# Optimization experiments

Hardware: AMD Instinct MI355X
Metric: run time of the kernel (lower is better)

## Reference

```python
import jax, jax.numpy as jnp
import numpy as np

B, F, C, W_, H_ = 4, 8, 256, 7, 7   # batch, frames, compressed channels (in_dim//r), width, height
CIN = 2048                          # in_dim
CH = CIN // 16                      # in_dim // (2*r) = 128, per-branch q/k channels


def _pw2d(x, W, b):
    # 1x1 Conv2d == per-pixel channel matmul. x: (N,Cin,H,W), W: (Cout,Cin)
    return jnp.einsum('nchw,oc->nohw', x, W) + b[None, :, None, None]


def setup_inputs() -> dict:
    key = jax.random.key(0)
    ks = iter(jax.random.split(key, 40))
    def rn(shape, s=0.02):
        return jax.random.normal(next(ks), shape, dtype=jnp.float32) * s
    inp = {
        'x':       rn((B * F, CIN, H_, W_), 1.0),
        'domainX': rn((B * F, CIN, H_, W_), 1.0),
        'domainY': rn((B * F, 1, H_, W_), 1.0),
        # conv1_1_pre (1 -> 2048), output is discarded in forward but computed faithfully
        'w_pre': rn((CIN, 1)), 'b_pre': rn((CIN,)),
        # conv3 (2048 -> 256); its weight is SHARED with layer1_downconv and layer1_downconv_Y
        'w_conv3': rn((C, CIN)), 'b_conv3': rn((C,)),
        # value_conv 1x1x1 Conv3d (256 -> 2048); weight SHARED with layer1_upconv(_Y)
        'w_value': rn((CIN, C)), 'b_value': rn((CIN,)),
        # tied-weight convs have their own biases
        'b_l1down': rn((C,)), 'b_l1up': rn((CIN,)),
        'b_l1down_Y': rn((C,)), 'b_l1up_Y': rn((CIN,)),
        # layer2 convs: independent weights (layer2_*gamma init to 0, so init add is a no-op)
        'w_l2down': rn((C, CIN)), 'b_l2down': rn((C,)),
        'w_l2up': rn((CIN, C)), 'b_l2up': rn((CIN,)),
        'w_l2down_Y': rn((C, CIN)), 'b_l2down_Y': rn((C,)),
        'w_l2up_Y': rn((CIN, C)), 'b_l2up_Y': rn((CIN,)),
        # q/k projections (2048 -> 128 each)
        'w_c11': rn((CH, CIN)), 'b_c11': rn((CH,)),
        'w_c12': rn((CH, CIN)), 'b_c12': rn((CH,)),
        'w_c21': rn((CH, CIN)), 'b_c21': rn((CH,)),
        'w_c22': rn((CH, CIN)), 'b_c22': rn((CH,)),
        'pos_embedV': rn((1, F, C * H_ * W_), 1.0),
        'gamma': jnp.asarray(0.01, dtype=jnp.float32),
    }
    return inp


def reference(x, domainX, domainY, w_pre, b_pre, w_conv3, b_conv3, w_value, b_value,
              b_l1down, b_l1up, b_l1down_Y, b_l1up_Y,
              w_l2down, b_l2down, w_l2up, b_l2up,
              w_l2down_Y, b_l2down_Y, w_l2up_Y, b_l2up_Y,
              w_c11, b_c11, w_c12, b_c12, w_c21, b_c21, w_c22, b_c22,
              pos_embedV, gamma):
    S = F * W_ * H_  # 392 tokens per clip
    # conv1_1_pre output is overwritten in the original forward (dead computation)
    _dead = _pw2d(domainY, w_pre, b_pre)
    del _dead
    # domainY path: down(conv3 weight) -> up(value_conv weight) -> layer2 down -> layer2 up
    # (create5D/create4D + permutes + 1x1x1 conv3d collapse to pointwise channel matmuls)
    dY = _pw2d(_pw2d(_pw2d(_pw2d(domainX, w_conv3, b_l1down_Y), w_value, b_l1up_Y),
                     w_l2down_Y, b_l2down_Y), w_l2up_Y, b_l2up_Y)
    q4 = jnp.concatenate([_pw2d(x, w_c11, b_c11), _pw2d(dY, w_c12, b_c12)], axis=1)  # (32,256,7,7)
    q = q4.reshape(B, F, C, W_, H_).transpose(0, 1, 3, 4, 2).reshape(B, S, C)
    # domainX path (same structure, shared layer1 weights, its own biases)
    dX = _pw2d(_pw2d(_pw2d(_pw2d(domainX, w_conv3, b_l1down), w_value, b_l1up),
                     w_l2down, b_l2down), w_l2up, b_l2up)
    k4 = jnp.concatenate([_pw2d(x, w_c21, b_c21), _pw2d(dX, w_c22, b_c22)], axis=1)
    k5 = k4.reshape(B, F, C, W_, H_).transpose(0, 1, 3, 4, 2)        # (B,F,W,H,C)
    k = k5.transpose(0, 2, 1, 3, 4).reshape(B, C, S)                 # faithful odd permute
    # value: conv3 -> +pos_embed -> rearrange to (B, S, C)
    v4 = _pw2d(x, w_conv3, b_conv3)                                  # (32,256,7,7)
    v = v4.reshape(B, F, C * W_ * H_) + pos_embedV                   # dropout p=0 is identity
    v = v.reshape(B, F, C, W_, H_).transpose(0, 1, 3, 4, 2).reshape(B, S, C)
    attn = jax.nn.softmax(jnp.einsum('bnc,bcm->bnm', q, k), axis=-1)  # (B,392,392)
    out = jnp.einsum('bnm,bmc->bnc', attn, v)
    out = out.reshape(B, F, W_, H_, C).transpose(0, 4, 1, 2, 3)      # (B,C,F,W,H)
    out = jnp.einsum('bcthw,oc->bothw', out, w_value) + b_value[None, :, None, None, None]
    out = out.transpose(0, 2, 1, 3, 4).reshape(B * F, CIN, W_, H_)
    return (gamma * out + x) * out + x
```

## Files before the change

kernel.cpp:

```cpp
#include <hip/hip_runtime.h>
#include <hip/hip_bf16.h>


typedef __attribute__((ext_vector_type(8))) _Float16 half8;
typedef __attribute__((ext_vector_type(4))) float f32x4;

#define TOKENS 1568

__device__ __forceinline__ ushort f2h(float f) {
    _Float16 h = (_Float16)f;
    return *(ushort*)&h;
}
__device__ __forceinline__ float h2f(ushort u) {
    _Float16 h = *(_Float16*)&u;
    return (float)h;
}

__device__ __forceinline__ void gl16(const void* g, void* l) {
    __builtin_amdgcn_global_load_lds(
        (const __attribute__((address_space(1))) unsigned int*)g,
        (__attribute__((address_space(3))) unsigned int*)l, 16, 0, 0);
}

#define EPI_PART  0
#define EPI_F16   1
#define EPI_QK2   2
#define EPI_FINAL 3

struct GA {
    const ushort* Ah; int lda; long sA;
    const ushort* Wh; int ldw; long sW;
    const float* bias; int sB;
    int nkc, Kc;
    float* fO; ushort* bO; ushort* bO2;
    int ldc; long sC; int M, N;
    int nx, ny;
    const float *ex, *gamma; float* fout;
};

template<int EPI>
__device__ __forceinline__ void gmm_body(const GA g, int bx, int by, int bzf,
                                         ushort* LA, ushort* LW)
{
    const int tid = threadIdx.x;
    const int bz = bzf / g.nkc;
    const int kc = bzf % g.nkc;
    const int row0 = by * 64, col0 = bx * 128;

    const int srow = tid >> 2;
    const int sq   = (tid & 3) ^ (srow & 3);
    int am  = row0 + srow;      if (am  > g.M - 1) am  = g.M - 1;
    int wn0 = col0 + srow;      if (wn0 > g.N - 1) wn0 = g.N - 1;
    int wn1 = col0 + 64 + srow; if (wn1 > g.N - 1) wn1 = g.N - 1;
    const long kbase = (long)kc * g.Kc + sq * 8;
    const ushort* gA  = g.Ah + bz * g.sA + (long)am  * g.lda + kbase;
    const ushort* gW0 = g.Wh + bz * g.sW + (long)wn0 * g.ldw + kbase;
    const ushort* gW1 = g.Wh + bz * g.sW + (long)wn1 * g.ldw + kbase;
    const int wb = (tid & 192) * 8;

    auto STAGE = [&](int buf, int k0) {
        gl16(gA + k0, LA + buf * 2048 + wb);
        gl16(gW0 + k0, LW + buf * 4096 + wb);
        gl16(gW1 + k0, LW + buf * 4096 + 2048 + wb);
    };

    const int lane = tid & 63, wv = tid >> 6;
    const int wr = (wv >> 1) * 32, wc = (wv & 1) * 64;
    const int fr = lane & 15;
    const int ksw = ((lane >> 4) ^ (lane & 3)) * 8;
    int aoff[2], boff[4];
#pragma unroll
    for (int mi = 0; mi < 2; ++mi) aoff[mi] = (wr + mi * 16 + fr) * 32 + ksw;
#pragma unroll
    for (int ni = 0; ni < 4; ++ni) boff[ni] = (wc + ni * 16 + fr) * 32 + ksw;

    f32x4 acc[2][4];
#pragma unroll
    for (int mi = 0; mi < 2; ++mi)
#pragma unroll
        for (int ni = 0; ni < 4; ++ni) acc[mi][ni] = (f32x4){0.f, 0.f, 0.f, 0.f};

    STAGE(0, 0);
    __syncthreads();
    int cur = 0;
    for (int k0 = 0; k0 < g.Kc; k0 += 32) {
        if (k0 + 32 < g.Kc) STAGE(cur ^ 1, k0 + 32);

        half8 fa[2], fb[4];
#pragma unroll
        for (int mi = 0; mi < 2; ++mi) fa[mi] = *(half8*)&LA[cur * 2048 + aoff[mi]];
#pragma unroll
        for (int ni = 0; ni < 4; ++ni) fb[ni] = *(half8*)&LW[cur * 4096 + boff[ni]];
#pragma unroll
        for (int mi = 0; mi < 2; ++mi)
#pragma unroll
            for (int ni = 0; ni < 4; ++ni)
                acc[mi][ni] = __builtin_amdgcn_mfma_f32_16x16x32_f16(fa[mi], fb[ni], acc[mi][ni], 0, 0, 0);
        __syncthreads();
        cur ^= 1;
    }

    const int q4 = (lane >> 4) * 4;
    float gg = 0.f;
    if constexpr (EPI == EPI_FINAL) gg = g.gamma[0];
#pragma unroll
    for (int mi = 0; mi < 2; ++mi)
#pragma unroll
        for (int ni = 0; ni < 4; ++ni)
#pragma unroll
            for (int qi = 0; qi < 4; ++qi) {
                int m = row0 + wr + mi * 16 + q4 + qi;
                int n = col0 + wc + ni * 16 + fr;
                if (m >= g.M || n >= g.N) continue;
                float v = acc[mi][ni][qi];
                if (g.bias) v += g.bias[bz * g.sB + n];
                if constexpr (EPI == EPI_PART) {
                    g.fO[(long)bzf * g.sC + (long)m * g.ldc + n] = v;
                } else if constexpr (EPI == EPI_F16) {
                    g.bO[(long)bzf * g.sC + (long)m * g.ldc + n] = f2h(v);
                } else if constexpr (EPI == EPI_QK2) {
                    ushort h = f2h(v);
                    if (n < 128) {
                        int c = 128 + n;
                        int p = m % 49, img = m / 49, f = img & 7, b = img >> 3;
                        int flat = (p / 7) * 14336 + f * 1792 + (p % 7) * 256 + c;
                        int ci = flat / 392, mm = flat % 392;
                        g.bO2[(long)b * 100352 + (long)mm * 256 + ci] = h;
                    } else {
                        g.bO[m * 256 + n] = h;
                    }
                } else {
                    int nimg = m / 49, p = m % 49;
                    long xi = (long)nimg * (2048 * 49) + (long)n * 49 + p;
                    float xv = g.ex[xi];
                    g.fout[xi] = (gg * v + xv) * v + xv;
                }
            }
}

template<int EPI>
__global__ __launch_bounds__(256)
void gmm(GA g)
{
    __shared__ __align__(16) ushort LA[2 * 2048], LW[2 * 4096];
    gmm_body<EPI>(g, blockIdx.x, blockIdx.y, blockIdx.z, LA, LW);
}

__global__ __launch_bounds__(256)
void gmm4(GA g1, int n1, GA g2, int n2, GA g3, int n3, GA g4)
{
    __shared__ __align__(16) ushort LA[2 * 2048], LW[2 * 4096];
    int id = blockIdx.x;
    if (id < n1) {
        int bx = id % g1.nx, t = id / g1.nx;
        gmm_body<EPI_PART>(g1, bx, t % g1.ny, t / g1.ny, LA, LW);
    } else if (id < n1 + n2) {
        id -= n1;
        int bx = id % g2.nx, t = id / g2.nx;
        gmm_body<EPI_PART>(g2, bx, t % g2.ny, t / g2.ny, LA, LW);
    } else if (id < n1 + n2 + n3) {
        id -= n1 + n2;
        int bx = id % g3.nx, t = id / g3.nx;
        gmm_body<EPI_PART>(g3, bx, t % g3.ny, t / g3.ny, LA, LW);
    } else {
        id -= n1 + n2 + n3;
        int bx = id % g4.nx, t = id / g4.nx;
        gmm_body<EPI_PART>(g4, bx, t % g4.ny, t / g4.ny, LA, LW);
    }
}

__global__ __launch_bounds__(256)
void prep(const float* c11, const float* c21, const float* conv3,
          const float* c22, const float* c12, const float* wval,
          const float* w2dX, const float* w2dY,
          const float* b_c11, const float* b_c21, const float* b_conv3,
          const float* x, const float* dX,
          const float* w2u, const float* w2uY, const float* wv,
          ushort* Wg1, ushort* C2, ushort* Wval, ushort* W2dS, float* bg1,
          ushort* Xt, ushort* DXt,
          ushort* W2uT, ushort* WvT)
{
    __shared__ float tile[64][65];
    int b = blockIdx.x;
    int tid = threadIdx.x;
    if (b < 12290) {
        int e = b * 256 + tid;
        if (e < 1048576) {
            float v = e < 262144 ? c11[e] : e < 524288 ? c21[e - 262144] : conv3[e - 524288];
            Wg1[e] = f2h(v);
        } else if (e < 1572864) {
            int i = e - 1048576;
            C2[i] = f2h(i < 262144 ? c22[i] : c12[i - 262144]);
        } else if (e < 2097152) {
            int i = e - 1572864; Wval[i] = f2h(wval[i]);
        } else if (e < 2097664) {
            int i = e - 2097152;
            bg1[i] = i < 128 ? b_c11[i] : i < 256 ? b_c21[i - 128] : b_conv3[i - 256];
        } else {
            int i = e - 2097664;
            W2dS[i] = f2h(i < 524288 ? w2dX[i] : w2dY[i - 524288]);
        }
    } else if (b < 14338) {
        int local = b - 12290;
        int z = local >> 10;
        int rem = local & 1023;
        int n = rem & 31, c0 = (rem >> 5) * 64;
        const float* src = z ? dX : x;
        ushort* oh = z ? DXt : Xt;
        const float* s = src + (long)n * (2048 * 49) + (long)c0 * 49;
        for (int idx = tid; idx < 64 * 49; idx += 256)
            tile[idx / 49][idx % 49] = s[idx];
        __syncthreads();
        for (int idx = tid; idx < 49 * 64; idx += 256) {
            int p = idx >> 6, cl = idx & 63;
            long o = (long)(n * 49 + p) * 2048 + c0 + cl;
            oh[o] = f2h(tile[cl][p]);
        }
    } else {
        int local = b - 14338;
        int zc = local >> 7, t = local & 127;
        const float* src; ushort* dh;
        switch (zc) {
            case 0:  src = w2u;  dh = W2uT;          break;
            case 1:  src = w2uY; dh = W2uT + 524288; break;
            default: src = wv;   dh = WvT;           break;
        }
        const int rows = 2048, cols = 256;
        int tilesX = cols >> 6;
        int tx = t % tilesX, ty = t / tilesX;
        for (int i = tid; i < 4096; i += 256) {
            int r = i >> 6, c = i & 63;
            tile[r][c] = src[(long)(ty * 64 + r) * cols + tx * 64 + c];
        }
        __syncthreads();
        for (int i = tid; i < 4096; i += 256) {
            int c = i >> 6, r = i & 63;
            long o = (long)(tx * 64 + c) * rows + ty * 64 + r;
            dh[o] = f2h(tile[r][c]);
        }
    }
}

__global__ __launch_bounds__(256)
void redA(const float* __restrict__ PG1, const float* __restrict__ bg1,
          const float* __restrict__ pos,
          ushort* Q, ushort* Km, ushort* V,
          const float* __restrict__ A1p, ushort* A1,
          const float* __restrict__ Dp, ushort* DT,
          const float* __restrict__ P0p, ushort* P0,
          const float* w2dX, const float* w2dY,
          const float* b1dX, const float* b1uX, const float* b2dX,
          const float* b1dY, const float* b1uY, const float* b2dY,
          float* __restrict__ dvec)
{
    int blk = blockIdx.x, tid = threadIdx.x;
    if (blk < 3136) {
        int idx = blk * 256 + tid;
        int m = idx >> 9, n = idx & 511;
        float v = bg1[n];
#pragma unroll
        for (int k = 0; k < 8; ++k) v += PG1[(long)k * 802816 + idx];
        int p = m % 49, img = m / 49;
        int f = img & 7, b = img >> 3;
        if (n < 128) {
            Q[m * 256 + n] = f2h(v);
        } else if (n < 256) {
            int c = n - 128;
            int flat = (p / 7) * 14336 + f * 1792 + (p % 7) * 256 + c;
            int ci = flat / 392, mm = flat % 392;
            Km[(long)b * 100352 + (long)mm * 256 + ci] = f2h(v);
        } else {
            int c = n - 256;
            v += pos[f * 12544 + c * 49 + p];
            int s = m % 392;
            long o = (long)b * 106496 + (long)c * 416 + s;
            V[o] = f2h(v);
            if (s < 24) V[o + 392] = 0;
        }
    } else if (blk < 3200) {
        int b2 = blk - 3136;
#pragma unroll
        for (int r = 0; r < 4; ++r) {
            int idx = b2 * 1024 + r * 256 + tid;
            int z = idx >> 15, e = idx & 32767;
            float v = 0.f;
#pragma unroll
            for (int k = 0; k < 8; ++k) v += A1p[(long)(z * 8 + k) * 32768 + e];
            A1[idx] = f2h(v);
        }
    } else if (blk < 3232) {
        int b2 = blk - 3200;
#pragma unroll
        for (int r = 0; r < 16; ++r) {
            int idx = b2 * 4096 + r * 256 + tid;
            int z = idx >> 16, e = idx & 65535;
            int i = e >> 8, j = e & 255;
            float v = 0.f;
#pragma unroll
            for (int k = 0; k < 8; ++k) v += Dp[(long)(z * 8 + k) * 65536 + e];
            DT[(long)z * 65536 + (long)j * 256 + i] = f2h(v);
        }
    } else if (blk < 3360) {
        int blk2 = blk - 3232;
        int z = blk2 >> 6;
        int lane = tid & 63, wv = tid >> 6;
        int c = (blk2 & 63) * 4 + wv;
        const float* w2d = (z ? w2dY : w2dX) + (long)c * 2048;
        const float* b1d = z ? b1dY : b1dX;
        const float* b1u = z ? b1uY : b1uX;
        const float* b2d = z ? b2dY : b2dX;
        float acc = 0.f;
        for (int o = lane; o < 2048; o += 64) acc = fmaf(w2d[o], b1u[o], acc);
        for (int j = lane; j < 256; j += 64) {
            float d = 0.f;
#pragma unroll
            for (int k = 0; k < 8; ++k) d += Dp[(long)(z * 8 + k) * 65536 + (long)c * 256 + j];
            acc = fmaf(d, b1d[j], acc);
        }
        for (int off = 32; off; off >>= 1) acc += __shfl_down(acc, off, 64);
        if (lane == 0) dvec[z * 256 + c] = acc + b2d[c];
    } else {
        int idx = (blk - 3360) * 256 + tid;
        float v = 0.f;
#pragma unroll
        for (int k = 0; k < 4; ++k) v += P0p[(long)k * 401408 + idx];
        P0[idx] = f2h(v);
    }
}

__global__ __launch_bounds__(256)
void a3kc(GA gA3,
          const ushort* __restrict__ A1, const float* __restrict__ dvec,
          const float* c22, const float* c12,
          const float* b2uX, const float* b2uY,
          const float* bc22, const float* bc12, float* kc)
{
    __shared__ __align__(16) ushort LA[2 * 2048], LW[2 * 4096];
    int id = blockIdx.x;
    if (id < 8) {
        int bx = id & 1, t = id >> 1;
        gmm_body<EPI_F16>(gA3, bx, t & 1, t >> 1, LA, LW);
        return;
    }
    int tid = threadIdx.x, lane = tid & 63, wv = tid >> 6;
    int w = (id - 8) * 4 + wv;
    int z = w >> 7, i = w & 127;
    const ushort* a1 = A1 + (long)z * 32768 + i * 256;
    const float* dv = dvec + z * 256;
    const float* cr = (z ? c12 : c22) + (long)i * 2048;
    const float* b2u = z ? b2uY : b2uX;
    float acc = 0.f;
    for (int c = lane; c < 256; c += 64) acc = fmaf(h2f(a1[c]), dv[c], acc);
    for (int o = lane; o < 2048; o += 64) acc = fmaf(cr[o], b2u[o], acc);
    for (int off = 32; off; off >>= 1) acc += __shfl_down(acc, off, 64);
    if (lane == 0) kc[z * 128 + i] = acc + (z ? bc12 : bc22)[i];
}

__global__ __launch_bounds__(256)
void fattn(const ushort* __restrict__ Qg, const ushort* __restrict__ Kmg,
           const ushort* __restrict__ VT, ushort* __restrict__ O)
{
    __shared__ float raw[16 * 420];
    __shared__ ushort P[16 * 424];
    const int b = blockIdx.y;
    const int r0 = blockIdx.x * 16;
    const int tid = threadIdx.x;
    const int lane = tid & 63, wv = tid >> 6;
    const int fr = lane & 15, g = lane >> 4;
    const int kb = g * 8;
    const long base = (long)b * 100352;
    const long vbase = (long)b * 106496;

    int qr = r0 + fr; if (qr > 391) qr = 391;
    const ushort* qp = Qg + base + (long)qr * 256 + kb;
    half8 qh[8];
#pragma unroll
    for (int kf = 0; kf < 8; ++kf) qh[kf] = *(const half8*)(qp + kf * 32);

    for (int nf = wv; nf < 26; nf += 4) {
        int kcol = nf * 16 + fr; if (kcol > 391) kcol = 391;
        const ushort* kp = Kmg + base + (long)kcol * 256 + kb;
        f32x4 a = (f32x4){0.f, 0.f, 0.f, 0.f};
#pragma unroll
        for (int kf = 0; kf < 8; ++kf) {
            half8 bh = *(const half8*)(kp + kf * 32);
            a = __builtin_amdgcn_mfma_f32_16x16x32_f16(qh[kf], bh, a, 0, 0, 0);
        }
#pragma unroll
        for (int q = 0; q < 4; ++q)
            raw[(g * 4 + q) * 420 + nf * 16 + fr] = a[q];
    }
    __syncthreads();

    {
        int row = tid >> 4, j = tid & 15;
        float v[26];
        float m = -1e30f;
#pragma unroll
        for (int k = 0; k < 26; ++k) {
            int col = j + 16 * k;
            v[k] = (col < 392) ? raw[row * 420 + col] : -1e30f;
            m = fmaxf(m, v[k]);
        }
#pragma unroll
        for (int off = 8; off; off >>= 1) m = fmaxf(m, __shfl_xor(m, off, 16));
        float s = 0.f;
#pragma unroll
        for (int k = 0; k < 26; ++k) { v[k] = __expf(v[k] - m); s += v[k]; }
#pragma unroll
        for (int off = 8; off; off >>= 1) s += __shfl_xor(s, off, 16);
        float inv = 1.f / s;
#pragma unroll
        for (int k = 0; k < 26; ++k) {
            int col = j + 16 * k;
            P[row * 424 + col] = (col < 392) ? f2h(v[k] * inv) : (ushort)0;
        }
    }
    __syncthreads();

    const int cf0 = wv * 4;
    f32x4 o[4];
#pragma unroll
    for (int c = 0; c < 4; ++c) o[c] = (f32x4){0.f, 0.f, 0.f, 0.f};
#pragma unroll
    for (int kf = 0; kf < 13; ++kf) {
        half8 pa = *(half8*)&P[fr * 424 + kf * 32 + kb];
#pragma unroll
        for (int c = 0; c < 4; ++c) {
            const ushort* vp = VT + vbase + (long)((cf0 + c) * 16 + fr) * 416 + kf * 32 + kb;
            half8 vb = *(const half8*)vp;
            o[c] = __builtin_amdgcn_mfma_f32_16x16x32_f16(pa, vb, o[c], 0, 0, 0);
        }
    }
#pragma unroll
    for (int c = 0; c < 4; ++c)
#pragma unroll
        for (int q = 0; q < 4; ++q) {
            int orow = r0 + g * 4 + q;
            if (orow < 392)
                O[base + (long)orow * 256 + (cf0 + c) * 16 + fr] = f2h(o[c][q]);
        }
}

extern "C" void kernel_launch(void* const* d_in, const int* in_sizes, int n_in,
                              void* d_out, int out_size, void* d_ws, size_t ws_size,
                              hipStream_t stream)
{
    const float* x        = (const float*)d_in[0];
    const float* domainX  = (const float*)d_in[1];
    const float* w_conv3  = (const float*)d_in[5];
    const float* b_conv3  = (const float*)d_in[6];
    const float* w_value  = (const float*)d_in[7];
    const float* b_value  = (const float*)d_in[8];
    const float* b_l1down   = (const float*)d_in[9];
    const float* b_l1up     = (const float*)d_in[10];
    const float* b_l1down_Y = (const float*)d_in[11];
    const float* b_l1up_Y   = (const float*)d_in[12];
    const float* w_l2down   = (const float*)d_in[13];
    const float* b_l2down   = (const float*)d_in[14];
    const float* w_l2up     = (const float*)d_in[15];
    const float* b_l2up     = (const float*)d_in[16];
    const float* w_l2down_Y = (const float*)d_in[17];
    const float* b_l2down_Y = (const float*)d_in[18];
    const float* w_l2up_Y   = (const float*)d_in[19];
    const float* b_l2up_Y   = (const float*)d_in[20];
    const float* w_c11 = (const float*)d_in[21];
    const float* b_c11 = (const float*)d_in[22];
    const float* w_c12 = (const float*)d_in[23];
    const float* b_c12 = (const float*)d_in[24];
    const float* w_c21 = (const float*)d_in[25];
    const float* b_c21 = (const float*)d_in[26];
    const float* w_c22 = (const float*)d_in[27];
    const float* b_c22 = (const float*)d_in[28];
    const float* pos   = (const float*)d_in[29];
    const float* gamma = (const float*)d_in[30];
    float* out = (float*)d_out;

    ushort* U = (ushort*)d_ws;
    float*  Fp = (float*)d_ws;

    const long oXt   = 0;
    const long oDXt  = 3211264;
    const long oWg1  = 6422528;
    const long oWval = 7471104;
    const long oC2   = 7995392;
    const long oW2uT = 8519680;
    const long oWvT  = 9568256;
    const long oW2dS = 10092544;
    const long oQ    = 11141120;
    const long oKm   = 11542528;
    const long oVT   = 11943936;
    const long oA1   = 12369920;
    const long oDT   = 12435456;
    const long oA3   = 12566528;
    const long oP0   = 12632064;
    const long oO    = 13033472;
    const long fPG1  = 6979584;
    const long fP0p  = 13402112;
    const long fA1p  = 15007744;
    const long fDp   = 15532032;
    const long fbg1  = 16580608;
    const long fkc   = 16581120;
    const long fdv   = 16581376;

    GA Z = {};

    prep<<<dim3(14722), 256, 0, stream>>>(
        w_c11, w_c21, w_conv3, w_c22, w_c12, w_value, w_l2down, w_l2down_Y,
        b_c11, b_c21, b_conv3, x, domainX,
        w_l2up, w_l2up_Y, w_value,
        U + oWg1, U + oC2, U + oWval, U + oW2dS, Fp + fbg1,
        U + oXt, U + oDXt,
        U + oW2uT, U + oWvT);

    {
        GA g1 = Z;
        g1.Ah = U + oXt; g1.lda = 2048; g1.sA = 0;
        g1.Wh = U + oWg1; g1.ldw = 2048; g1.sW = 0;
        g1.nkc = 8; g1.Kc = 256; g1.fO = Fp + fPG1;
        g1.ldc = 512; g1.sC = 802816; g1.M = TOKENS; g1.N = 512; g1.nx = 4; g1.ny = 25;
        GA ga1 = Z;
        ga1.Ah = U + oC2; ga1.lda = 2048; ga1.sA = 262144;
        ga1.Wh = U + oW2uT; ga1.ldw = 2048; ga1.sW = 524288;
        ga1.nkc = 8; ga1.Kc = 256; ga1.fO = Fp + fA1p;
        ga1.ldc = 256; ga1.sC = 32768; ga1.M = 128; ga1.N = 256; ga1.nx = 2; ga1.ny = 2;
        GA gd = Z;
        gd.Ah = U + oW2dS; gd.lda = 2048; gd.sA = 524288;
        gd.Wh = U + oWvT; gd.ldw = 2048; gd.sW = 0;
        gd.nkc = 8; gd.Kc = 256; gd.fO = Fp + fDp;
        gd.ldc = 256; gd.sC = 65536; gd.M = 256; gd.N = 256; gd.nx = 2; gd.ny = 4;
        GA gp = Z;
        gp.Ah = U + oDXt; gp.lda = 2048; gp.sA = 0;
        gp.Wh = U + oWg1 + 524288; gp.ldw = 2048; gp.sW = 0;
        gp.nkc = 4; gp.Kc = 512; gp.fO = Fp + fP0p;
        gp.ldc = 256; gp.sC = 401408; gp.M = TOKENS; gp.N = 256; gp.nx = 2; gp.ny = 25;
        gmm4<<<dim3(1192), 256, 0, stream>>>(g1, 800, ga1, 64, gd, 128, gp);
    }

    redA<<<dim3(4928), 256, 0, stream>>>(Fp + fPG1, Fp + fbg1, pos,
        U + oQ, U + oKm, U + oVT,
        Fp + fA1p, U + oA1,
        Fp + fDp, U + oDT,
        Fp + fP0p, U + oP0,
        w_l2down, w_l2down_Y,
        b_l1down, b_l1up, b_l2down,
        b_l1down_Y, b_l1up_Y, b_l2down_Y,
        Fp + fdv);

    {
        GA g = Z;
        g.Ah = U + oA1; g.lda = 256; g.sA = 32768;
        g.Wh = U + oDT; g.ldw = 256; g.sW = 65536;
        g.nkc = 1; g.Kc = 256; g.bO = U + oA3;
        g.ldc = 256; g.sC = 32768; g.M = 128; g.N = 256; g.nx = 2; g.ny = 2;
        a3kc<<<dim3(72), 256, 0, stream>>>(g,
            U + oA1, Fp + fdv,
            w_c22, w_c12, b_l2up, b_l2up_Y,
            b_c22, b_c12, Fp + fkc);
    }

    {
        GA g = Z;
        g.Ah = U + oP0; g.lda = 256; g.sA = 0;
        g.Wh = U + oA3; g.ldw = 256; g.sW = 0;
        g.bias = Fp + fkc; g.sB = 0;
        g.nkc = 1; g.Kc = 256;
        g.bO = U + oQ; g.bO2 = U + oKm;
        g.ldc = 0; g.sC = 0; g.M = TOKENS; g.N = 256; g.nx = 2; g.ny = 25;
        gmm<EPI_QK2><<<dim3(2, 25, 1), 256, 0, stream>>>(g);
    }

    fattn<<<dim3(25, 4), 256, 0, stream>>>(U + oQ, U + oKm, U + oVT, U + oO);

    {
        GA g = Z;
        g.Ah = U + oO; g.lda = 256; g.sA = 0;
        g.Wh = U + oWval; g.ldw = 256; g.sW = 0;
        g.bias = b_value; g.sB = 0;
        g.nkc = 1; g.Kc = 256;
        g.ldc = 0; g.sC = 0; g.M = TOKENS; g.N = 2048; g.nx = 16; g.ny = 25;
        g.ex = x; g.gamma = gamma; g.fout = out;
        gmm<EPI_FINAL><<<dim3(16, 25, 1), 256, 0, stream>>>(g);
    }
}
```

Before: 147.8 us.

## Load GEMM fragments directly from global memory, dropping LDS staging

Removes the double-buffered LDS staging (global_load_lds plus barriers) from the shared GEMM body. Each lane now reads its MFMA A and B fragments straight from global memory. This drops the LDS allocation, so occupancy can rise, and eliminates the per-iteration __syncthreads. The cost is that no data is shared between waves: each wave re-fetches the tiles others also use, global accesses become less coalesced (16 B per row per lane), and load latency is no longer overlapped with compute by prefetch.

Result: slower. 174.3 us (+17.9%).

```diff
diff --git a/kernel.cpp b/kernel.cpp
--- a/kernel.cpp
+++ b/kernel.cpp
@@ -14,12 +14,6 @@
 __device__ __forceinline__ float h2f(ushort u) {
     _Float16 h = *(_Float16*)&u;
     return (float)h;
-}
-
-__device__ __forceinline__ void gl16(const void* g, void* l) {
-    __builtin_amdgcn_global_load_lds(
-        (const __attribute__((address_space(1))) unsigned int*)g,
-        (__attribute__((address_space(3))) unsigned int*)l, 16, 0, 0);
 }
 
 #define EPI_PART  0
@@ -39,40 +33,31 @@
 };
 
 template<int EPI>
-__device__ __forceinline__ void gmm_body(const GA g, int bx, int by, int bzf,
-                                         ushort* LA, ushort* LW)
+__device__ __forceinline__ void gmm_body(const GA g, int bx, int by, int bzf)
 {
     const int tid = threadIdx.x;
     const int bz = bzf / g.nkc;
     const int kc = bzf % g.nkc;
     const int row0 = by * 64, col0 = bx * 128;
 
-    const int srow = tid >> 2;
-    const int sq   = (tid & 3) ^ (srow & 3);
-    int am  = row0 + srow;      if (am  > g.M - 1) am  = g.M - 1;
-    int wn0 = col0 + srow;      if (wn0 > g.N - 1) wn0 = g.N - 1;
-    int wn1 = col0 + 64 + srow; if (wn1 > g.N - 1) wn1 = g.N - 1;
-    const long kbase = (long)kc * g.Kc + sq * 8;
-    const ushort* gA  = g.Ah + bz * g.sA + (long)am  * g.lda + kbase;
-    const ushort* gW0 = g.Wh + bz * g.sW + (long)wn0 * g.ldw + kbase;
-    const ushort* gW1 = g.Wh + bz * g.sW + (long)wn1 * g.ldw + kbase;
-    const int wb = (tid & 192) * 8;
-
-    auto STAGE = [&](int buf, int k0) {
-        gl16(gA + k0, LA + buf * 2048 + wb);
-        gl16(gW0 + k0, LW + buf * 4096 + wb);
-        gl16(gW1 + k0, LW + buf * 4096 + 2048 + wb);
-    };
-
     const int lane = tid & 63, wv = tid >> 6;
     const int wr = (wv >> 1) * 32, wc = (wv & 1) * 64;
     const int fr = lane & 15;
-    const int ksw = ((lane >> 4) ^ (lane & 3)) * 8;
-    int aoff[2], boff[4];
-#pragma unroll
-    for (int mi = 0; mi < 2; ++mi) aoff[mi] = (wr + mi * 16 + fr) * 32 + ksw;
-#pragma unroll
-    for (int ni = 0; ni < 4; ++ni) boff[ni] = (wc + ni * 16 + fr) * 32 + ksw;
+    const int kb = (lane >> 4) * 8;
+    const long kbase = (long)kc * g.Kc + kb;
+
+    const ushort* pa[2];
+#pragma unroll
+    for (int mi = 0; mi < 2; ++mi) {
+        int r = row0 + wr + mi * 16 + fr; if (r > g.M - 1) r = g.M - 1;
+        pa[mi] = g.Ah + bz * g.sA + (long)r * g.lda + kbase;
+    }
+    const ushort* pb[4];
+#pragma unroll
+    for (int ni = 0; ni < 4; ++ni) {
+        int c = col0 + wc + ni * 16 + fr; if (c > g.N - 1) c = g.N - 1;
+        pb[ni] = g.Wh + bz * g.sW + (long)c * g.ldw + kbase;
+    }
 
     f32x4 acc[2][4];
 #pragma unroll
@@ -80,24 +65,17 @@
 #pragma unroll
         for (int ni = 0; ni < 4; ++ni) acc[mi][ni] = (f32x4){0.f, 0.f, 0.f, 0.f};
 
-    STAGE(0, 0);
-    __syncthreads();
-    int cur = 0;
     for (int k0 = 0; k0 < g.Kc; k0 += 32) {
-        if (k0 + 32 < g.Kc) STAGE(cur ^ 1, k0 + 32);
-
         half8 fa[2], fb[4];
 #pragma unroll
-        for (int mi = 0; mi < 2; ++mi) fa[mi] = *(half8*)&LA[cur * 2048 + aoff[mi]];
-#pragma unroll
-        for (int ni = 0; ni < 4; ++ni) fb[ni] = *(half8*)&LW[cur * 4096 + boff[ni]];
+        for (int mi = 0; mi < 2; ++mi) fa[mi] = *(const half8*)(pa[mi] + k0);
+#pragma unroll
+        for (int ni = 0; ni < 4; ++ni) fb[ni] = *(const half8*)(pb[ni] + k0);
 #pragma unroll
         for (int mi = 0; mi < 2; ++mi)
 #pragma unroll
             for (int ni = 0; ni < 4; ++ni)
                 acc[mi][ni] = __builtin_amdgcn_mfma_f32_16x16x32_f16(fa[mi], fb[ni], acc[mi][ni], 0, 0, 0);
-        __syncthreads();
-        cur ^= 1;
     }
 
     const int q4 = (lane >> 4) * 4;
@@ -142,30 +120,28 @@
 __global__ __launch_bounds__(256)
 void gmm(GA g)
 {
-    __shared__ __align__(16) ushort LA[2 * 2048], LW[2 * 4096];
-    gmm_body<EPI>(g, blockIdx.x, blockIdx.y, blockIdx.z, LA, LW);
+    gmm_body<EPI>(g, blockIdx.x, blockIdx.y, blockIdx.z);
 }
 
 __global__ __launch_bounds__(256)
 void gmm4(GA g1, int n1, GA g2, int n2, GA g3, int n3, GA g4)
 {
-    __shared__ __align__(16) ushort LA[2 * 2048], LW[2 * 4096];
     int id = blockIdx.x;
     if (id < n1) {
         int bx = id % g1.nx, t = id / g1.nx;
-        gmm_body<EPI_PART>(g1, bx, t % g1.ny, t / g1.ny, LA, LW);
+        gmm_body<EPI_PART>(g1, bx, t % g1.ny, t / g1.ny);
     } else if (id < n1 + n2) {
         id -= n1;
         int bx = id % g2.nx, t = id / g2.nx;
-        gmm_body<EPI_PART>(g2, bx, t % g2.ny, t / g2.ny, LA, LW);
+        gmm_body<EPI_PART>(g2, bx, t % g2.ny, t / g2.ny);
     } else if (id < n1 + n2 + n3) {
         id -= n1 + n2;
         int bx = id % g3.nx, t = id / g3.nx;
-        gmm_body<EPI_PART>(g3, bx, t % g3.ny, t / g3.ny, LA, LW);
+        gmm_body<EPI_PART>(g3, bx, t % g3.ny, t / g3.ny);
     } else {
         id -= n1 + n2 + n3;
         int bx = id % g4.nx, t = id / g4.nx;
-        gmm_body<EPI_PART>(g4, bx, t % g4.ny, t / g4.ny, LA, LW);
+        gmm_body<EPI_PART>(g4, bx, t % g4.ny, t / g4.ny);
     }
 }
 
@@ -335,11 +311,10 @@
           const float* b2uX, const float* b2uY,
           const float* bc22, const float* bc12, float* kc)
 {
-    __shared__ __align__(16) ushort LA[2 * 2048], LW[2 * 4096];
     int id = blockIdx.x;
     if (id < 8) {
         int bx = id & 1, t = id >> 1;
-        gmm_body<EPI_F16>(gA3, bx, t & 1, t >> 1, LA, LW);
+        gmm_body<EPI_F16>(gA3, bx, t & 1, t >> 1);
         return;
     }
     int tid = threadIdx.x, lane = tid & 63, wv = tid >> 6;
```

## Triple-buffer GEMM LDS staging with explicit vmcnt waits

Applied to the files above, without the earlier changes.

Replaces the double-buffered K loop with a three-stage ring of LDS buffers. Two tiles are prefetched ahead using global_load_lds, and explicit s_waitcnt vmcnt counts let the loop wait only for the oldest tile instead of draining all loads each iteration. This is meant to hide global load latency behind the MFMA work. In exchange, LDS use per block grows by half, which can lower occupancy, and correctness depends on the hardcoded vmcnt values matching the number of loads STAGE issues.

Result: no change. 150.4 us (+1.7%).

```diff
diff --git a/kernel.cpp b/kernel.cpp
--- a/kernel.cpp
+++ b/kernel.cpp
@@ -80,12 +80,22 @@
 #pragma unroll
         for (int ni = 0; ni < 4; ++ni) acc[mi][ni] = (f32x4){0.f, 0.f, 0.f, 0.f};
 
+    const int n = g.Kc >> 5;
     STAGE(0, 0);
-    __syncthreads();
-    int cur = 0;
-    for (int k0 = 0; k0 < g.Kc; k0 += 32) {
-        if (k0 + 32 < g.Kc) STAGE(cur ^ 1, k0 + 32);
-
+    STAGE(1, 32);
+    for (int it = 0; it < n; ++it) {
+        __builtin_amdgcn_s_barrier();
+        if (it + 2 < n) {
+            STAGE((it + 2) % 3, (it + 2) * 32);
+            asm volatile("s_waitcnt vmcnt(6)" ::: "memory");
+        } else if (it + 1 < n) {
+            asm volatile("s_waitcnt vmcnt(3)" ::: "memory");
+        } else {
+            asm volatile("s_waitcnt vmcnt(0)" ::: "memory");
+        }
+        __builtin_amdgcn_s_barrier();
+
+        const int cur = it % 3;
         half8 fa[2], fb[4];
 #pragma unroll
         for (int mi = 0; mi < 2; ++mi) fa[mi] = *(half8*)&LA[cur * 2048 + aoff[mi]];
@@ -96,8 +106,6 @@
 #pragma unroll
             for (int ni = 0; ni < 4; ++ni)
                 acc[mi][ni] = __builtin_amdgcn_mfma_f32_16x16x32_f16(fa[mi], fb[ni], acc[mi][ni], 0, 0, 0);
-        __syncthreads();
-        cur ^= 1;
     }
 
     const int q4 = (lane >> 4) * 4;
@@ -110,28 +118,28 @@
 #pragma unroll
             for (int qi = 0; qi < 4; ++qi) {
                 int m = row0 + wr + mi * 16 + q4 + qi;
-                int n = col0 + wc + ni * 16 + fr;
-                if (m >= g.M || n >= g.N) continue;
+                int nn = col0 + wc + ni * 16 + fr;
+                if (m >= g.M || nn >= g.N) continue;
                 float v = acc[mi][ni][qi];
-                if (g.bias) v += g.bias[bz * g.sB + n];
+                if (g.bias) v += g.bias[bz * g.sB + nn];
                 if constexpr (EPI == EPI_PART) {
-                    g.fO[(long)bzf * g.sC + (long)m * g.ldc + n] = v;
+                    g.fO[(long)bzf * g.sC + (long)m * g.ldc + nn] = v;
                 } else if constexpr (EPI == EPI_F16) {
-                    g.bO[(long)bzf * g.sC + (long)m * g.ldc + n] = f2h(v);
+                    g.bO[(long)bzf * g.sC + (long)m * g.ldc + nn] = f2h(v);
                 } else if constexpr (EPI == EPI_QK2) {
                     ushort h = f2h(v);
-                    if (n < 128) {
-                        int c = 128 + n;
+                    if (nn < 128) {
+                        int c = 128 + nn;
                         int p = m % 49, img = m / 49, f = img & 7, b = img >> 3;
                         int flat = (p / 7) * 14336 + f * 1792 + (p % 7) * 256 + c;
                         int ci = flat / 392, mm = flat % 392;
                         g.bO2[(long)b * 100352 + (long)mm * 256 + ci] = h;
                     } else {
-                        g.bO[m * 256 + n] = h;
+                        g.bO[m * 256 + nn] = h;
                     }
                 } else {
                     int nimg = m / 49, p = m % 49;
-                    long xi = (long)nimg * (2048 * 49) + (long)n * 49 + p;
+                    long xi = (long)nimg * (2048 * 49) + (long)nn * 49 + p;
                     float xv = g.ex[xi];
                     g.fout[xi] = (gg * v + xv) * v + xv;
                 }
@@ -142,14 +150,14 @@
 __global__ __launch_bounds__(256)
 void gmm(GA g)
 {
-    __shared__ __align__(16) ushort LA[2 * 2048], LW[2 * 4096];
+    __shared__ __align__(16) ushort LA[3 * 2048], LW[3 * 4096];
     gmm_body<EPI>(g, blockIdx.x, blockIdx.y, blockIdx.z, LA, LW);
 }
 
 __global__ __launch_bounds__(256)
 void gmm4(GA g1, int n1, GA g2, int n2, GA g3, int n3, GA g4)
 {
-    __shared__ __align__(16) ushort LA[2 * 2048], LW[2 * 4096];
+    __shared__ __align__(16) ushort LA[3 * 2048], LW[3 * 4096];
     int id = blockIdx.x;
     if (id < n1) {
         int bx = id % g1.nx, t = id / g1.nx;
@@ -335,7 +343,7 @@
           const float* b2uX, const float* b2uY,
           const float* bc22, const float* bc12, float* kc)
 {
-    __shared__ __align__(16) ushort LA[2 * 2048], LW[2 * 4096];
+    __shared__ __align__(16) ushort LA[3 * 2048], LW[3 * 4096];
     int id = blockIdx.x;
     if (id < 8) {
         int bx = id & 1, t = id >> 1;
```
